# Optimization experiments

Measured on AMD Instinct MI355X. Metric: run time of the kernel, lower is better.

Reference implementation:

```python
import jax, jax.numpy as jnp
import numpy as np

N_HEAD = 16
NEG_INF = -1e9


def setup_inputs() -> dict:
    key = jax.random.key(0)
    ks = jax.random.split(key, 5)
    B, T, C = 2, 2048, 1024
    scale = 1.0 / np.sqrt(C)
    return {
        "x": jax.random.normal(ks[0], (B, T, C), dtype=jnp.float32),
        "wq": jax.random.normal(ks[1], (C, C), dtype=jnp.float32) * scale,
        "bq": jnp.zeros((C,), dtype=jnp.float32),
        "wk": jax.random.normal(ks[2], (C, C), dtype=jnp.float32) * scale,
        "bk": jnp.zeros((C,), dtype=jnp.float32),
        "wv": jax.random.normal(ks[3], (C, C), dtype=jnp.float32) * scale,
        "bv": jnp.zeros((C,), dtype=jnp.float32),
        "wo": jax.random.normal(ks[4], (C, C), dtype=jnp.float32) * scale,
        "bo": jnp.zeros((C,), dtype=jnp.float32),
    }


def reference(x, wq, bq, wk, bk, wv, bv, wo, bo):
    B, T, C = x.shape
    H = N_HEAD
    d = C // H
    # linear projections, split into heads: [B, T, H, d]
    q = (x @ wq + bq).reshape(B, T, H, d)
    k = (x @ wk + bk).reshape(B, T, H, d)
    v = (x @ wv + bv).reshape(B, T, H, d)
    # scaled dot-product attention scores: [B, H, Tq, Tk]
    scores = jnp.einsum("bqhd,bkhd->bhqk", q, k) / jnp.sqrt(jnp.float32(d))
    # causal mask: triu(diagonal=1) positions are masked out
    causal = jnp.triu(jnp.ones((T, T), dtype=bool), k=1)
    scores = jnp.where(causal[None, None, :, :], NEG_INF, scores)
    attn = jax.nn.softmax(scores, axis=-1)
    # weighted values, merge heads: [B, T, C]
    out = jnp.einsum("bhqk,bkhd->bqhd", attn, v).reshape(B, T, C)
    # output projection (dropout is identity in eval / p=0)
    return out @ wo + bo
```

## Files before the change

kernel.cpp:

```cpp
#include <hip/hip_runtime.h>
#include <cstdint>
#include <type_traits>


#define TSEQ  2048
#define BATCH 2
#define CDIM  1024
#define NHEAD 16
#define DHEAD 64
#define NROWS (BATCH * TSEQ)

#define QSCALE 0.1803368801111244f

typedef unsigned short u16;
typedef u16   u16x8  __attribute__((ext_vector_type(8)));
typedef __bf16 bf16x8 __attribute__((ext_vector_type(8)));
typedef __bf16 bf16x2 __attribute__((ext_vector_type(2)));
typedef float f32x4  __attribute__((ext_vector_type(4)));

typedef const __attribute__((address_space(1))) void* gas_vp;
typedef __attribute__((address_space(3))) void* las_vp;

__device__ __forceinline__ u16 f2bf(float f) {
  return __builtin_bit_cast(u16, (__bf16)f);
}

__device__ __forceinline__ uint32_t pack2bf(float a, float b) {
  bf16x2 v;
  v[0] = (__bf16)a;
  v[1] = (__bf16)b;
  return __builtin_bit_cast(uint32_t, v);
}

__device__ __forceinline__ f32x4 mfma_bf16(u16x8 a, u16x8 b, f32x4 c) {
  return __builtin_amdgcn_mfma_f32_16x16x32_bf16(
      __builtin_bit_cast(bf16x8, a), __builtin_bit_cast(bf16x8, b), c, 0, 0, 0);
}

__device__ __forceinline__ void gload16(const u16* g, u16* l) {
  __builtin_amdgcn_global_load_lds((gas_vp)g, (las_vp)l, 16, 0, 0);
}


__global__ __launch_bounds__(256) void cast_x_kernel(const float* __restrict__ in,
                                                     u16* __restrict__ out, int n4) {
  int i = blockIdx.x * 256 + threadIdx.x;
  if (i < n4) {
    float4 v = ((const float4*)in)[i];
    ((uint2*)out)[i] = make_uint2(pack2bf(v.x, v.y), pack2bf(v.z, v.w));
  }
}

__global__ __launch_bounds__(256) void transpose_cast_kernel(
    const float* __restrict__ w0, const float* __restrict__ w1,
    const float* __restrict__ w2, const float* __restrict__ w3,
    u16* __restrict__ outQKV, u16* __restrict__ outO) {
  __shared__ float tile[32][33];
  const int m = blockIdx.z;
  const float* w = (m == 0) ? w0 : (m == 1) ? w1 : (m == 2) ? w2 : w3;
  const float scale = (m == 0) ? QSCALE : 1.0f;
  u16* out = (m < 3) ? (outQKV + (size_t)m * CDIM * CDIM) : outO;
  const int n0 = blockIdx.x * 32;
  const int k0 = blockIdx.y * 32;
  const int tx = threadIdx.x, ty = threadIdx.y;
#pragma unroll
  for (int i = 0; i < 4; ++i)
    tile[ty + i * 8][tx] = w[(size_t)(k0 + ty + i * 8) * CDIM + n0 + tx];
  __syncthreads();
#pragma unroll
  for (int i = 0; i < 4; ++i)
    out[(size_t)(n0 + ty + i * 8) * CDIM + k0 + tx] = f2bf(tile[tx][ty + i * 8] * scale);
}

__global__ __launch_bounds__(256) void bias_concat_kernel(const float* __restrict__ bq,
                                                          const float* __restrict__ bk,
                                                          const float* __restrict__ bv,
                                                          float* __restrict__ out) {
  int i = blockIdx.x * 256 + threadIdx.x;
  if (i < 3 * CDIM) {
    float v = (i < CDIM) ? bq[i] * QSCALE
            : (i < 2 * CDIM) ? bk[i - CDIM] : bv[i - 2 * CDIM];
    out[i] = v;
  }
}

__global__ __launch_bounds__(256) void vtrans_kernel(const u16* __restrict__ QKV,
                                                     u16* __restrict__ Vt) {
  __shared__ u16 tile[32][33];
  const int bh = blockIdx.z;
  const int b = bh >> 4, h = bh & 15;
  const int t0 = blockIdx.x * 32, d0 = blockIdx.y * 32;
  const int tx = threadIdx.x, ty = threadIdx.y;
#pragma unroll
  for (int i = 0; i < 4; ++i)
    tile[ty + i * 8][tx] =
        QKV[(size_t)(b * TSEQ + t0 + ty + i * 8) * (3 * CDIM) + 2 * CDIM + h * DHEAD + d0 + tx];
  __syncthreads();
#pragma unroll
  for (int i = 0; i < 4; ++i)
    Vt[(size_t)((b * NHEAD + h) * DHEAD + d0 + ty + i * 8) * TSEQ + t0 + tx] =
        tile[tx][ty + i * 8];
}


template <typename OutT>
__global__ __launch_bounds__(256) void gemm_bt_kernel(
    const u16* __restrict__ A, const u16* __restrict__ Bt,
    const float* __restrict__ bias, OutT* __restrict__ C,
    int M, int N, int K, int mblocks) {
  __shared__ u16 As[128 * 32];
  __shared__ u16 Bs[128 * 32];
  const int nwg = gridDim.x;
  const int lid = blockIdx.x;
  const int swz = (lid & 7) * (nwg >> 3) + (lid >> 3);
  const int m0 = (swz % mblocks) * 128;
  const int n0 = (swz / mblocks) * 128;

  const int t = threadIdx.x;
  const int lane = t & 63;
  const int w = t >> 6;
  const int wr = w >> 1, wc = w & 1;
  const int l15 = lane & 15;
  const int lg = lane >> 4;
  const int srow = lane >> 2;
  const int scol = (lane & 3) * 8;

  f32x4 acc[4][4];
#pragma unroll
  for (int i = 0; i < 4; ++i)
#pragma unroll
    for (int j = 0; j < 4; ++j) acc[i][j] = f32x4{0.f, 0.f, 0.f, 0.f};

  for (int k0 = 0; k0 < K; k0 += 32) {
    __syncthreads();
#pragma unroll
    for (int ci = 0; ci < 2; ++ci) {
      const int chunk = w * 2 + ci;
      const int grow = chunk * 16 + srow;
      gload16(&A[(size_t)(m0 + grow) * K + k0 + scol], &As[chunk * 512]);
      gload16(&Bt[(size_t)(n0 + grow) * K + k0 + scol], &Bs[chunk * 512]);
    }
    __syncthreads();
    u16x8 af[4], bf[4];
#pragma unroll
    for (int i = 0; i < 4; ++i)
      af[i] = *(const u16x8*)(&As[(wr * 64 + i * 16 + l15) * 32 + lg * 8]);
#pragma unroll
    for (int j = 0; j < 4; ++j)
      bf[j] = *(const u16x8*)(&Bs[(wc * 64 + j * 16 + l15) * 32 + lg * 8]);
#pragma unroll
    for (int i = 0; i < 4; ++i)
#pragma unroll
      for (int j = 0; j < 4; ++j) acc[i][j] = mfma_bf16(af[i], bf[j], acc[i][j]);
  }

#pragma unroll
  for (int j = 0; j < 4; ++j) {
    int col = n0 + wc * 64 + j * 16 + l15;
    float bv = bias[col];
#pragma unroll
    for (int i = 0; i < 4; ++i) {
#pragma unroll
      for (int r = 0; r < 4; ++r) {
        int row = m0 + wr * 64 + i * 16 + lg * 4 + r;
        float val = acc[i][j][r] + bv;
        if constexpr (std::is_same<OutT, float>::value)
          C[(size_t)row * N + col] = val;
        else
          C[(size_t)row * N + col] = f2bf(val);
      }
    }
  }
}


__global__ __launch_bounds__(512) void attn_kernel(const u16* __restrict__ QKV,
                                                   const u16* __restrict__ Vt,
                                                   u16* __restrict__ O) {
  constexpr int LDK = 72;
  __shared__ u16 Ks[64 * LDK];
  __shared__ u16 Vs[64 * LDK];
  __shared__ u16 Ps[8 * 16 * LDK];

  const int t = threadIdx.x;
  const int lane = t & 63;
  const int w = t >> 6;
  const int l15 = lane & 15, lg = lane >> 4;

  const int lid = blockIdx.x;
  const int xcd = lid & 7;
  const int m = lid >> 3;
  const int bh = (m & 3) * 8 + xcd;
  const int qt = 15 - (m >> 2);
  const int b = bh >> 4, h = bh & 15;
  const int q0 = qt * 128;
  const int qrow = q0 + w * 16;
  const int nkt = (qt + 1) * 2;

  const size_t RS = 3 * CDIM;
  const u16* Qp  = QKV + (size_t)(b * TSEQ) * RS + h * DHEAD;
  const u16* Kp  = Qp + CDIM;
  const u16* Vgp = Vt + (size_t)(b * NHEAD + h) * DHEAD * TSEQ;
  u16* Pw = &Ps[w * 16 * LDK];

  u16x8 qf[2];
#pragma unroll
  for (int c = 0; c < 2; ++c)
    qf[c] = *(const u16x8*)(&Qp[(size_t)(qrow + l15) * RS + c * 32 + lg * 8]);

  f32x4 acc[4];
#pragma unroll
  for (int g = 0; g < 4; ++g) acc[g] = f32x4{0.f, 0.f, 0.f, 0.f};
  float m_run = -3e38f, l_run = 0.f;

  const int srow = t >> 3;
  const int scc = (t & 7) * 8;

  u16x8 kreg = *(const u16x8*)(&Kp[(size_t)srow * RS + scc]);
  u16x8 vreg = *(const u16x8*)(&Vgp[(size_t)srow * TSEQ + scc]);

  for (int kb = 0; kb < nkt; ++kb) {
    __syncthreads();
    *(u16x8*)(&Ks[srow * LDK + scc]) = kreg;
    *(u16x8*)(&Vs[srow * LDK + scc]) = vreg;
    __syncthreads();

    if (kb + 1 < nkt) {
      kreg = *(const u16x8*)(&Kp[(size_t)((kb + 1) * 64 + srow) * RS + scc]);
      vreg = *(const u16x8*)(&Vgp[(size_t)srow * TSEQ + (kb + 1) * 64 + scc]);
    }

    f32x4 sfr[4];
    __builtin_amdgcn_s_setprio(1);
#pragma unroll
    for (int f = 0; f < 4; ++f) {
      f32x4 s = f32x4{0.f, 0.f, 0.f, 0.f};
#pragma unroll
      for (int c = 0; c < 2; ++c) {
        u16x8 kf = *(const u16x8*)(&Ks[(f * 16 + l15) * LDK + c * 32 + lg * 8]);
        s = mfma_bf16(kf, qf[c], s);
      }
      sfr[f] = s;
    }
    __builtin_amdgcn_s_setprio(0);

    if (kb * 64 + 63 > qrow) {
      const int q_abs = qrow + l15;
#pragma unroll
      for (int f = 0; f < 4; ++f) {
        const int kbase = kb * 64 + f * 16 + lg * 4;
#pragma unroll
        for (int r = 0; r < 4; ++r)
          if (kbase + r > q_abs) sfr[f][r] = -1e9f;
      }
    }

    float mx = sfr[0][0];
#pragma unroll
    for (int f = 0; f < 4; ++f)
#pragma unroll
      for (int r = 0; r < 4; ++r) mx = fmaxf(mx, sfr[f][r]);

    if (__any(mx > m_run + 8.f)) {
      float gm = mx;
      gm = fmaxf(gm, __shfl_xor(gm, 16));
      gm = fmaxf(gm, __shfl_xor(gm, 32));
      float mnew = fmaxf(m_run, gm);
      float fac = exp2f(m_run - mnew);
      m_run = mnew;
      l_run *= fac;
#pragma unroll
      for (int g = 0; g < 4; ++g) acc[g] *= fac;
    }

    float ls = 0.f;
#pragma unroll
    for (int f = 0; f < 4; ++f) {
      float p0 = exp2f(sfr[f][0] - m_run);
      float p1 = exp2f(sfr[f][1] - m_run);
      float p2 = exp2f(sfr[f][2] - m_run);
      float p3 = exp2f(sfr[f][3] - m_run);
      ls += (p0 + p1) + (p2 + p3);
      int base = (l15) * LDK + f * 16 + lg * 4;
      *(uint32_t*)(&Pw[base]) = pack2bf(p0, p1);
      *(uint32_t*)(&Pw[base + 2]) = pack2bf(p2, p3);
    }
    l_run += ls;

    __builtin_amdgcn_s_setprio(1);
#pragma unroll
    for (int c = 0; c < 2; ++c) {
      u16x8 pf = *(const u16x8*)(&Pw[(l15) * LDK + c * 32 + lg * 8]);
#pragma unroll
      for (int g = 0; g < 4; ++g) {
        u16x8 vf = *(const u16x8*)(&Vs[(g * 16 + l15) * LDK + c * 32 + lg * 8]);
        acc[g] = mfma_bf16(vf, pf, acc[g]);
      }
    }
    __builtin_amdgcn_s_setprio(0);
  }

  float lt = l_run;
  lt += __shfl_xor(lt, 16);
  lt += __shfl_xor(lt, 32);
  float inv = 1.f / lt;
#pragma unroll
  for (int g = 0; g < 4; ++g) {
    int base = (l15) * LDK + g * 16 + lg * 4;
    *(uint32_t*)(&Pw[base]) = pack2bf(acc[g][0] * inv, acc[g][1] * inv);
    *(uint32_t*)(&Pw[base + 2]) = pack2bf(acc[g][2] * inv, acc[g][3] * inv);
  }
#pragma unroll
  for (int i = 0; i < 2; ++i) {
    int rl = i * 8 + (lane >> 3);
    int cc = (lane & 7) * 8;
    u16x8 vv = *(const u16x8*)(&Pw[rl * LDK + cc]);
    *(u16x8*)(&O[(size_t)(b * TSEQ + qrow + rl) * CDIM + h * DHEAD + cc]) = vv;
  }
}


extern "C" void kernel_launch(void* const* d_in, const int* in_sizes, int n_in,
                              void* d_out, int out_size, void* d_ws, size_t ws_size,
                              hipStream_t stream) {
  const float* x  = (const float*)d_in[0];
  const float* wq = (const float*)d_in[1];
  const float* bq = (const float*)d_in[2];
  const float* wk = (const float*)d_in[3];
  const float* bk = (const float*)d_in[4];
  const float* wv = (const float*)d_in[5];
  const float* bv = (const float*)d_in[6];
  const float* wo = (const float*)d_in[7];
  const float* bo = (const float*)d_in[8];
  float* out = (float*)d_out;

  char* ws = (char*)d_ws;
  u16*  xb      = (u16*)(ws);
  u16*  Vtg     = (u16*)(ws);
  u16*  wqkvT   = (u16*)(ws + (8ll << 20));
  u16*  woT     = (u16*)(ws + (14ll << 20));
  u16*  QKV     = (u16*)(ws + (16ll << 20));
  u16*  Obuf    = (u16*)(ws + (40ll << 20));
  float* biasqkv = (float*)(ws + (48ll << 20));

  cast_x_kernel<<<(NROWS * CDIM / 4 + 255) / 256, 256, 0, stream>>>(x, xb, NROWS * CDIM / 4);
  {
    dim3 g(CDIM / 32, CDIM / 32, 4), blk(32, 8);
    transpose_cast_kernel<<<g, blk, 0, stream>>>(wq, wk, wv, wo, wqkvT, woT);
  }
  bias_concat_kernel<<<12, 256, 0, stream>>>(bq, bk, bv, biasqkv);
  gemm_bt_kernel<u16><<<(NROWS / 128) * ((3 * CDIM) / 128), 256, 0, stream>>>(
      xb, wqkvT, biasqkv, QKV, NROWS, 3 * CDIM, CDIM, NROWS / 128);
  {
    dim3 g(TSEQ / 32, DHEAD / 32, BATCH * NHEAD), blk(32, 8);
    vtrans_kernel<<<g, blk, 0, stream>>>(QKV, Vtg);
  }
  attn_kernel<<<512, 512, 0, stream>>>(QKV, Vtg, Obuf);
  gemm_bt_kernel<float><<<(NROWS / 128) * (CDIM / 128), 256, 0, stream>>>(
      Obuf, woT, bo, out, NROWS, CDIM, CDIM, NROWS / 128);
}
```

Measured before the change: 138.1 us.

## Rewrite attention with 32x32 MFMA tiles, register P via permlane, swizzled LDS

The attention kernel moves from 16x16x32 to 32x32x16 bf16 MFMAs, with 4 waves each owning 32 query rows instead of 8 waves owning 16. The probability tile now stays in registers, reshuffled with v_permlane32_swap instead of going through an LDS round trip. K and V tiles use an XOR-swizzled LDS layout without padding. Waves whose rows are fully masked skip the tile. This is meant to cut LDS traffic and MFMA issue count, at the cost of fewer waves per block and more register pressure.

Result: no change. 140.3 us (+1.6%).

```diff
diff --git a/kernel.cpp b/kernel.cpp
--- a/kernel.cpp
+++ b/kernel.cpp
@@ -17,6 +17,8 @@
 typedef __bf16 bf16x8 __attribute__((ext_vector_type(8)));
 typedef __bf16 bf16x2 __attribute__((ext_vector_type(2)));
 typedef float f32x4  __attribute__((ext_vector_type(4)));
+typedef float f32x16 __attribute__((ext_vector_type(16)));
+typedef uint32_t u32x4 __attribute__((ext_vector_type(4)));
 
 typedef const __attribute__((address_space(1))) void* gas_vp;
 typedef __attribute__((address_space(3))) void* las_vp;
@@ -35,6 +37,15 @@
 __device__ __forceinline__ f32x4 mfma_bf16(u16x8 a, u16x8 b, f32x4 c) {
   return __builtin_amdgcn_mfma_f32_16x16x32_bf16(
       __builtin_bit_cast(bf16x8, a), __builtin_bit_cast(bf16x8, b), c, 0, 0, 0);
+}
+
+__device__ __forceinline__ f32x16 mfma32(u16x8 a, u16x8 b, f32x16 c) {
+  return __builtin_amdgcn_mfma_f32_32x32x16_bf16(
+      __builtin_bit_cast(bf16x8, a), __builtin_bit_cast(bf16x8, b), c, 0, 0, 0);
+}
+
+__device__ __forceinline__ void perm32swap(uint32_t& a, uint32_t& b) {
+  asm volatile("v_permlane32_swap_b32 %0, %1" : "+v"(a), "+v"(b));
 }
 
 __device__ __forceinline__ void gload16(const u16* g, u16* l) {
@@ -174,148 +185,174 @@
 }
 
 
-__global__ __launch_bounds__(512) void attn_kernel(const u16* __restrict__ QKV,
+__global__ __launch_bounds__(256) void attn_kernel(const u16* __restrict__ QKV,
                                                    const u16* __restrict__ Vt,
                                                    u16* __restrict__ O) {
-  constexpr int LDK = 72;
-  __shared__ u16 Ks[64 * LDK];
-  __shared__ u16 Vs[64 * LDK];
-  __shared__ u16 Ps[8 * 16 * LDK];
+  __shared__ u16 KV[2][64 * 64];
+  char* KsB = (char*)KV[0];
+  char* VsB = (char*)KV[1];
 
   const int t = threadIdx.x;
   const int lane = t & 63;
   const int w = t >> 6;
-  const int l15 = lane & 15, lg = lane >> 4;
+  const int l31 = lane & 31;
+  const int hi = lane >> 5;
+  const int xorv = (l31 & 7) << 4;
 
   const int lid = blockIdx.x;
   const int xcd = lid & 7;
   const int m = lid >> 3;
   const int bh = (m & 3) * 8 + xcd;
-  const int qt = 15 - (m >> 2);
+  const int qb = 15 - (m >> 2);
   const int b = bh >> 4, h = bh & 15;
-  const int q0 = qt * 128;
-  const int qrow = q0 + w * 16;
-  const int nkt = (qt + 1) * 2;
+  const int q0w = qb * 128 + w * 32;
+  const int nkt = (qb + 1) * 2;
 
   const size_t RS = 3 * CDIM;
   const u16* Qp  = QKV + (size_t)(b * TSEQ) * RS + h * DHEAD;
   const u16* Kp  = Qp + CDIM;
   const u16* Vgp = Vt + (size_t)(b * NHEAD + h) * DHEAD * TSEQ;
-  u16* Pw = &Ps[w * 16 * LDK];
-
-  u16x8 qf[2];
-#pragma unroll
-  for (int c = 0; c < 2; ++c)
-    qf[c] = *(const u16x8*)(&Qp[(size_t)(qrow + l15) * RS + c * 32 + lg * 8]);
-
-  f32x4 acc[4];
-#pragma unroll
-  for (int g = 0; g < 4; ++g) acc[g] = f32x4{0.f, 0.f, 0.f, 0.f};
+
+  u16x8 qf[4];
+#pragma unroll
+  for (int c = 0; c < 4; ++c)
+    qf[c] = *(const u16x8*)(&Qp[(size_t)(q0w + l31) * RS + c * 16 + hi * 8]);
+
+  f32x16 acc0, acc1;
+#pragma unroll
+  for (int i = 0; i < 16; ++i) { acc0[i] = 0.f; acc1[i] = 0.f; }
   float m_run = -3e38f, l_run = 0.f;
 
-  const int srow = t >> 3;
-  const int scc = (t & 7) * 8;
-
-  u16x8 kreg = *(const u16x8*)(&Kp[(size_t)srow * RS + scc]);
-  u16x8 vreg = *(const u16x8*)(&Vgp[(size_t)srow * TSEQ + scc]);
+  const int sr = t >> 2;
+  const int sc0 = (t & 3) * 16;
+  const int swb0 = sr * 128 + ((sc0 * 2) ^ ((sr & 7) << 4));
+  const int swb1 = sr * 128 + ((sc0 * 2 + 16) ^ ((sr & 7) << 4));
+
+  u16x8 kreg0 = *(const u16x8*)(&Kp[(size_t)sr * RS + sc0]);
+  u16x8 kreg1 = *(const u16x8*)(&Kp[(size_t)sr * RS + sc0 + 8]);
+  u16x8 vreg0 = *(const u16x8*)(&Vgp[(size_t)sr * TSEQ + sc0]);
+  u16x8 vreg1 = *(const u16x8*)(&Vgp[(size_t)sr * TSEQ + sc0 + 8]);
 
   for (int kb = 0; kb < nkt; ++kb) {
     __syncthreads();
-    *(u16x8*)(&Ks[srow * LDK + scc]) = kreg;
-    *(u16x8*)(&Vs[srow * LDK + scc]) = vreg;
+    *(u16x8*)(KsB + swb0) = kreg0;
+    *(u16x8*)(KsB + swb1) = kreg1;
+    *(u16x8*)(VsB + swb0) = vreg0;
+    *(u16x8*)(VsB + swb1) = vreg1;
     __syncthreads();
 
     if (kb + 1 < nkt) {
-      kreg = *(const u16x8*)(&Kp[(size_t)((kb + 1) * 64 + srow) * RS + scc]);
-      vreg = *(const u16x8*)(&Vgp[(size_t)srow * TSEQ + (kb + 1) * 64 + scc]);
-    }
-
-    f32x4 sfr[4];
+      kreg0 = *(const u16x8*)(&Kp[(size_t)((kb + 1) * 64 + sr) * RS + sc0]);
+      kreg1 = *(const u16x8*)(&Kp[(size_t)((kb + 1) * 64 + sr) * RS + sc0 + 8]);
+      vreg0 = *(const u16x8*)(&Vgp[(size_t)sr * TSEQ + (kb + 1) * 64 + sc0]);
+      vreg1 = *(const u16x8*)(&Vgp[(size_t)sr * TSEQ + (kb + 1) * 64 + sc0 + 8]);
+    }
+
+    if (kb * 64 > q0w + 31) continue;
+
+    f32x16 s0, s1;
+#pragma unroll
+    for (int i = 0; i < 16; ++i) { s0[i] = 0.f; s1[i] = 0.f; }
     __builtin_amdgcn_s_setprio(1);
 #pragma unroll
-    for (int f = 0; f < 4; ++f) {
-      f32x4 s = f32x4{0.f, 0.f, 0.f, 0.f};
-#pragma unroll
-      for (int c = 0; c < 2; ++c) {
-        u16x8 kf = *(const u16x8*)(&Ks[(f * 16 + l15) * LDK + c * 32 + lg * 8]);
-        s = mfma_bf16(kf, qf[c], s);
+    for (int c = 0; c < 4; ++c) {
+      const int boff = (c * 32 + hi * 16) ^ xorv;
+      u16x8 ka = *(const u16x8*)(KsB + l31 * 128 + boff);
+      u16x8 kc = *(const u16x8*)(KsB + (32 + l31) * 128 + boff);
+      s0 = mfma32(ka, qf[c], s0);
+      s1 = mfma32(kc, qf[c], s1);
+    }
+    __builtin_amdgcn_s_setprio(0);
+
+    if (kb * 64 + 63 > q0w) {
+      const int q_abs = q0w + l31;
+#pragma unroll
+      for (int r = 0; r < 16; ++r) {
+        const int crow = (r & 3) + 8 * (r >> 2) + 4 * hi;
+        if (kb * 64 + crow > q_abs) s0[r] = -1e9f;
+        if (kb * 64 + 32 + crow > q_abs) s1[r] = -1e9f;
       }
-      sfr[f] = s;
-    }
-    __builtin_amdgcn_s_setprio(0);
-
-    if (kb * 64 + 63 > qrow) {
-      const int q_abs = qrow + l15;
-#pragma unroll
-      for (int f = 0; f < 4; ++f) {
-        const int kbase = kb * 64 + f * 16 + lg * 4;
-#pragma unroll
-        for (int r = 0; r < 4; ++r)
-          if (kbase + r > q_abs) sfr[f][r] = -1e9f;
-      }
-    }
-
-    float mx = sfr[0][0];
-#pragma unroll
-    for (int f = 0; f < 4; ++f)
-#pragma unroll
-      for (int r = 0; r < 4; ++r) mx = fmaxf(mx, sfr[f][r]);
-
+    }
+
+    float mx = s0[0];
+#pragma unroll
+    for (int r = 0; r < 16; ++r) { mx = fmaxf(mx, s0[r]); mx = fmaxf(mx, s1[r]); }
     if (__any(mx > m_run + 8.f)) {
-      float gm = mx;
-      gm = fmaxf(gm, __shfl_xor(gm, 16));
-      gm = fmaxf(gm, __shfl_xor(gm, 32));
+      float gm = fmaxf(mx, __shfl_xor(mx, 32));
       float mnew = fmaxf(m_run, gm);
       float fac = exp2f(m_run - mnew);
       m_run = mnew;
       l_run *= fac;
 #pragma unroll
-      for (int g = 0; g < 4; ++g) acc[g] *= fac;
-    }
-
+      for (int i = 0; i < 16; ++i) { acc0[i] *= fac; acc1[i] *= fac; }
+    }
+
+    uint32_t P2a[8], P2b[8];
     float ls = 0.f;
 #pragma unroll
-    for (int f = 0; f < 4; ++f) {
-      float p0 = exp2f(sfr[f][0] - m_run);
-      float p1 = exp2f(sfr[f][1] - m_run);
-      float p2 = exp2f(sfr[f][2] - m_run);
-      float p3 = exp2f(sfr[f][3] - m_run);
+    for (int j = 0; j < 8; ++j) {
+      float p0 = exp2f(s0[2 * j] - m_run);
+      float p1 = exp2f(s0[2 * j + 1] - m_run);
+      float p2 = exp2f(s1[2 * j] - m_run);
+      float p3 = exp2f(s1[2 * j + 1] - m_run);
       ls += (p0 + p1) + (p2 + p3);
-      int base = (l15) * LDK + f * 16 + lg * 4;
-      *(uint32_t*)(&Pw[base]) = pack2bf(p0, p1);
-      *(uint32_t*)(&Pw[base + 2]) = pack2bf(p2, p3);
+      P2a[j] = pack2bf(p0, p1);
+      P2b[j] = pack2bf(p2, p3);
     }
     l_run += ls;
 
+    u16x8 pf0, pf1, pf2, pf3;
+    {
+      uint32_t a0 = P2a[0], b0 = P2a[2], a1 = P2a[1], b1 = P2a[3];
+      perm32swap(a0, b0);
+      perm32swap(a1, b1);
+      pf0 = __builtin_bit_cast(u16x8, u32x4{a0, a1, b0, b1});
+      uint32_t c0 = P2a[4], d0 = P2a[6], c1 = P2a[5], d1 = P2a[7];
+      perm32swap(c0, d0);
+      perm32swap(c1, d1);
+      pf1 = __builtin_bit_cast(u16x8, u32x4{c0, c1, d0, d1});
+      uint32_t e0 = P2b[0], f0 = P2b[2], e1 = P2b[1], f1 = P2b[3];
+      perm32swap(e0, f0);
+      perm32swap(e1, f1);
+      pf2 = __builtin_bit_cast(u16x8, u32x4{e0, e1, f0, f1});
+      uint32_t g0 = P2b[4], h0 = P2b[6], g1 = P2b[5], h1 = P2b[7];
+      perm32swap(g0, h0);
+      perm32swap(g1, h1);
+      pf3 = __builtin_bit_cast(u16x8, u32x4{g0, g1, h0, h1});
+    }
+
     __builtin_amdgcn_s_setprio(1);
 #pragma unroll
-    for (int c = 0; c < 2; ++c) {
-      u16x8 pf = *(const u16x8*)(&Pw[(l15) * LDK + c * 32 + lg * 8]);
-#pragma unroll
-      for (int g = 0; g < 4; ++g) {
-        u16x8 vf = *(const u16x8*)(&Vs[(g * 16 + l15) * LDK + c * 32 + lg * 8]);
-        acc[g] = mfma_bf16(vf, pf, acc[g]);
-      }
+    for (int ks = 0; ks < 4; ++ks) {
+      const int boff = (ks * 32 + hi * 16) ^ xorv;
+      u16x8 va = *(const u16x8*)(VsB + l31 * 128 + boff);
+      u16x8 vb = *(const u16x8*)(VsB + (32 + l31) * 128 + boff);
+      u16x8 pf = (ks == 0) ? pf0 : (ks == 1) ? pf1 : (ks == 2) ? pf2 : pf3;
+      acc0 = mfma32(va, pf, acc0);
+      acc1 = mfma32(vb, pf, acc1);
     }
     __builtin_amdgcn_s_setprio(0);
   }
 
-  float lt = l_run;
-  lt += __shfl_xor(lt, 16);
-  lt += __shfl_xor(lt, 32);
+  __syncthreads();
+
+  float lt = l_run + __shfl_xor(l_run, 32);
   float inv = 1.f / lt;
-#pragma unroll
-  for (int g = 0; g < 4; ++g) {
-    int base = (l15) * LDK + g * 16 + lg * 4;
-    *(uint32_t*)(&Pw[base]) = pack2bf(acc[g][0] * inv, acc[g][1] * inv);
-    *(uint32_t*)(&Pw[base + 2]) = pack2bf(acc[g][2] * inv, acc[g][3] * inv);
-  }
-#pragma unroll
-  for (int i = 0; i < 2; ++i) {
-    int rl = i * 8 + (lane >> 3);
-    int cc = (lane & 7) * 8;
-    u16x8 vv = *(const u16x8*)(&Pw[rl * LDK + cc]);
-    *(u16x8*)(&O[(size_t)(b * TSEQ + qrow + rl) * CDIM + h * DHEAD + cc]) = vv;
+  char* ob = (char*)KV[0] + w * 4096;
+#pragma unroll
+  for (int j = 0; j < 8; ++j) {
+    const int d0 = ((2 * j) & 3) + 8 * (j >> 1) + 4 * hi;
+    uint32_t pa = pack2bf(acc0[2 * j] * inv, acc0[2 * j + 1] * inv);
+    uint32_t pb = pack2bf(acc1[2 * j] * inv, acc1[2 * j + 1] * inv);
+    *(uint32_t*)(ob + l31 * 128 + ((d0 * 2) ^ ((l31 & 7) << 4))) = pa;
+    *(uint32_t*)(ob + l31 * 128 + (((32 + d0) * 2) ^ ((l31 & 7) << 4))) = pb;
+  }
+#pragma unroll
+  for (int i = 0; i < 4; ++i) {
+    const int rl = i * 8 + (lane >> 3);
+    const int ch = lane & 7;
+    u16x8 vv = *(const u16x8*)(ob + rl * 128 + ((ch * 16) ^ ((rl & 7) << 4)));
+    *(u16x8*)(&O[(size_t)(b * TSEQ + q0w + rl) * CDIM + h * DHEAD + ch * 8]) = vv;
   }
 }
 
@@ -355,7 +392,7 @@
     dim3 g(TSEQ / 32, DHEAD / 32, BATCH * NHEAD), blk(32, 8);
     vtrans_kernel<<<g, blk, 0, stream>>>(QKV, Vtg);
   }
-  attn_kernel<<<512, 512, 0, stream>>>(QKV, Vtg, Obuf);
+  attn_kernel<<<512, 256, 0, stream>>>(QKV, Vtg, Obuf);
   gemm_bt_kernel<float><<<(NROWS / 128) * (CDIM / 128), 256, 0, stream>>>(
       Obuf, woT, bo, out, NROWS, CDIM, CDIM, NROWS / 128);
 }
```
